# Kernel optimization log

Hardware: AMD Instinct MI355X
Metric: run time of the kernel (lower is better)

## Reference

```python
import jax, jax.numpy as jnp
import numpy as np

EPS = 1e-6

def _ln(x, g, b):
    mu = jnp.mean(x, axis=-1, keepdims=True)
    var = jnp.mean(jnp.square(x - mu), axis=-1, keepdims=True)
    return (x - mu) * jax.lax.rsqrt(var + EPS) * g + b

def setup_inputs() -> dict:
    key = jax.random.key(0)
    ks = jax.random.split(key, 8)
    B, S, D, H, HD, F = 4, 1024, 1024, 16, 64, 4096
    s = 0.02
    return {
        "hidden_state": jax.random.normal(ks[0], (B, S, D), jnp.float32),
        "mask": jnp.ones((B, S), jnp.int32),
        "Wq": jax.random.normal(ks[1], (H, D, HD), jnp.float32) * s,
        "bq": jnp.zeros((H, HD), jnp.float32),
        "Wk": jax.random.normal(ks[2], (H, D, HD), jnp.float32) * s,
        "bk": jnp.zeros((H, HD), jnp.float32),
        "Wv": jax.random.normal(ks[3], (H, D, HD), jnp.float32) * s,
        "bv": jnp.zeros((H, HD), jnp.float32),
        "Wo": jax.random.normal(ks[4], (D, D), jnp.float32) * s,
        "bo": jnp.zeros((D,), jnp.float32),
        "ln1_g": jnp.ones((D,), jnp.float32),
        "ln1_b": jnp.zeros((D,), jnp.float32),
        "ln2_g": jnp.ones((D,), jnp.float32),
        "ln2_b": jnp.zeros((D,), jnp.float32),
        "W1": jax.random.normal(ks[5], (D, F), jnp.float32) * s,
        "b1": jnp.zeros((F,), jnp.float32),
        "W2": jax.random.normal(ks[6], (F, D), jnp.float32) * s,
        "b2": jnp.zeros((D,), jnp.float32),
    }

def reference(hidden_state, mask, Wq, bq, Wk, bk, Wv, bv, Wo, bo,
              ln1_g, ln1_b, ln2_g, ln2_b, W1, b1, W2, b2):
    # Pre-norm
    x1 = _ln(hidden_state, ln1_g, ln1_b)  # [B,S,D]
    # Per-head projections stacked over head axis h
    q = jnp.einsum('bsd,hdk->bhsk', x1, Wq) + bq[:, None, :]
    k = jnp.einsum('bsd,hdk->bhsk', x1, Wk) + bk[:, None, :]
    v = jnp.einsum('bsd,hdk->bhsk', x1, Wv) + bv[:, None, :]
    head_dim = q.shape[-1]
    scores = jnp.einsum('bhqk,bhsk->bhqs', q, k) / jnp.sqrt(jnp.float32(head_dim))
    scores = jnp.where(mask[:, None, None, :] == 0, jnp.float32(-1e9), scores)
    w = jax.nn.softmax(scores, axis=-1)
    attn = jnp.einsum('bhqs,bhsk->bhqk', w, v)  # [B,H,S,HD]
    B, H, S, HD = attn.shape
    attn = attn.transpose(0, 2, 1, 3).reshape(B, S, H * HD)  # concat heads
    attn = attn @ Wo + bo
    h = attn + hidden_state
    x2 = _ln(h, ln2_g, ln2_b)
    ff = jax.nn.gelu(x2 @ W1 + b1, approximate=False) @ W2 + b2
    return ff + h
```

## Files before the change

### kernel.cpp

```cpp
#include <hip/hip_runtime.h>

typedef __bf16 bf16;
typedef __bf16 bf16x4 __attribute__((ext_vector_type(4)));
typedef __bf16 bf16x8 __attribute__((ext_vector_type(8)));
typedef float  f32x4  __attribute__((ext_vector_type(4)));

#define F32X4_ZERO ((f32x4){0.f, 0.f, 0.f, 0.f})

__device__ __forceinline__ f32x4 mfma16(bf16x8 a, bf16x8 b, f32x4 c) {
  return __builtin_amdgcn_mfma_f32_16x16x32_bf16(a, b, c, 0, 0, 0);
}

__device__ __forceinline__ void gld16(const void* g, void* l) {
  __builtin_amdgcn_global_load_lds((const __attribute__((address_space(1))) void*)g,
                                   (__attribute__((address_space(3))) void*)l, 16, 0, 0);
}

__device__ __forceinline__ float gelu_f(float u) {
  return 0.5f * u * (1.0f + erff(u * 0.70710678118654752f));
}

__device__ __forceinline__ bf16x8 frag_ld(const bf16* base, int row, int c16) {
  return *(const bf16x8*)((const char*)base + row * 128 + (((c16) ^ (row & 7)) << 4));
}

__device__ __forceinline__ bf16x8 frag_ld32(const bf16* base, int row, int c16) {
  return *(const bf16x8*)((const char*)base + row * 64 + ((c16 ^ ((row >> 1) & 3)) << 4));
}
#define WAITB(N) asm volatile("s_waitcnt vmcnt(" #N ")\ns_barrier" ::: "memory")

__global__ void transpose2(const float* __restrict__ src, size_t sBatch, int sStride,
                           bf16* __restrict__ dst, size_t dBatch, int dStride) {
  __shared__ bf16 t[32][33];
  src += (size_t)blockIdx.z * sBatch;
  dst += (size_t)blockIdx.z * dBatch;
  int c0 = blockIdx.x * 32, r0 = blockIdx.y * 32;
#pragma unroll
  for (int i = 0; i < 4; i++) {
    int r = threadIdx.y + i * 8;
    t[r][threadIdx.x] = (bf16)src[(size_t)(r0 + r) * sStride + c0 + threadIdx.x];
  }
  __syncthreads();
#pragma unroll
  for (int i = 0; i < 4; i++) {
    int c = threadIdx.y + i * 8;
    dst[(size_t)(c0 + c) * dStride + r0 + threadIdx.x] = t[threadIdx.x][c];
  }
}

__global__ __launch_bounds__(256) void ln_rows(const float* __restrict__ in,
                                               const float* __restrict__ gam,
                                               const float* __restrict__ bet,
                                               bf16* __restrict__ out) {
  int row = blockIdx.x, tid = threadIdx.x;
  f32x4 x = *(const f32x4*)(in + (size_t)row * 1024 + tid * 4);
  float s = 0.f, q = 0.f;
#pragma unroll
  for (int j = 0; j < 4; j++) { s += x[j]; q += x[j] * x[j]; }
#pragma unroll
  for (int o = 1; o < 64; o <<= 1) {
    s += __shfl_xor(s, o, 64);
    q += __shfl_xor(q, o, 64);
  }
  __shared__ float red[8];
  if ((tid & 63) == 0) { red[(tid >> 6) * 2] = s; red[(tid >> 6) * 2 + 1] = q; }
  __syncthreads();
  s = red[0] + red[2] + red[4] + red[6];
  q = red[1] + red[3] + red[5] + red[7];
  float mean = s * (1.f / 1024.f);
  float var  = q * (1.f / 1024.f) - mean * mean;
  float inv  = rsqrtf(var + 1e-6f);
  bf16x4 o;
#pragma unroll
  for (int j = 0; j < 4; j++) {
    int c = tid * 4 + j;
    o[j] = (bf16)((x[j] - mean) * inv * gam[c] + bet[c]);
  }
  *(bf16x4*)(out + (size_t)row * 1024 + tid * 4) = o;
}


__global__ __launch_bounds__(512) void pipe256_gelu(
    const bf16* __restrict__ A, const bf16* __restrict__ BT, const float* __restrict__ bias,
    int N, bf16* __restrict__ outb) {
  int tid = threadIdx.x, lane = tid & 63, wv = tid >> 6;
  int bid = blockIdx.x + (blockIdx.y << 4);
  int xcd = bid & 7, idx = bid >> 3;
  int m0 = ((xcd >> 1) * 4 + (idx >> 3)) * 256;
  int n0 = ((xcd & 1) * 8 + (idx & 7)) * 256;
  int wrow = (wv >> 2) * 128, wcol = (wv & 3) * 64;
  __shared__ __align__(16) bf16 lds[4][16384];
  f32x4 acc[8][4];
#pragma unroll
  for (int a = 0; a < 8; a++)
#pragma unroll
    for (int n = 0; n < 4; n++) acc[a][n] = F32X4_ZERO;

  constexpr int K = 1024, nk = K / 32;
  int rin = lane >> 2;
  int sbc = ((lane & 3) ^ ((lane >> 3) & 3)) * 16;
  auto stage = [&](int slot, int k0) {
#pragma unroll
    for (int j = 0; j < 4; j++) {
      int c = wv * 4 + j;
      if (c < 16)
        gld16((const char*)A + ((size_t)(m0 + c * 16 + rin) * K + k0) * 2 + sbc,
              (char*)lds[slot] + c * 1024);
      else
        gld16((const char*)BT + ((size_t)(n0 + (c - 16) * 16 + rin) * K + k0) * 2 + sbc,
              (char*)lds[slot] + c * 1024);
    }
  };

  stage(0, 0); stage(1, 32); stage(2, 64);
#pragma unroll 1
  for (int t = 0; t < nk; t++) {
    if (t < nk - 2)       WAITB(8);
    else if (t == nk - 2) WAITB(4);
    else                  WAITB(0);
    if (t + 3 < nk) stage((t + 3) & 3, (t + 3) * 32);
    const bf16* As = lds[t & 3];
    const bf16* Bs = lds[t & 3] + 8192;
    int c16 = lane >> 4;
    bf16x8 bfr[4];
#pragma unroll
    for (int nf = 0; nf < 4; nf++)
      bfr[nf] = frag_ld32(Bs, wcol + nf * 16 + (lane & 15), c16);
    __builtin_amdgcn_s_setprio(1);
#pragma unroll
    for (int mf = 0; mf < 8; mf++) {
      bf16x8 af = frag_ld32(As, wrow + mf * 16 + (lane & 15), c16);
#pragma unroll
      for (int nf = 0; nf < 4; nf++)
        acc[mf][nf] = mfma16(af, bfr[nf], acc[mf][nf]);
    }
    __builtin_amdgcn_s_setprio(0);
  }
#pragma unroll
  for (int mf = 0; mf < 8; mf++)
#pragma unroll
    for (int nf = 0; nf < 4; nf++)
#pragma unroll
      for (int i = 0; i < 4; i++) {
        int row = m0 + wrow + mf * 16 + ((lane >> 4) << 2) + i;
        int col = n0 + wcol + nf * 16 + (lane & 15);
        outb[(size_t)row * N + col] = (bf16)gelu_f(acc[mf][nf][i] + bias[col]);
      }
}

enum { EPI_WO = 0, EPI_GELU = 1, EPI_ACC0 = 2, EPI_ACC = 3, EPI_FINAL = 4 };

template <int EPI, int K>
__global__ __launch_bounds__(256) void pipe128(
    const bf16* __restrict__ A, const bf16* __restrict__ BT, const float* __restrict__ bias,
    int N,
    const float* __restrict__ resid, float* __restrict__ facc,
    bf16* __restrict__ outb, float* __restrict__ outf) {
  int tid = threadIdx.x, lane = tid & 63, wv = tid >> 6;
  int bid = blockIdx.x + (blockIdx.y << 3);
  int xcd = bid & 7, idx = bid >> 3;
  int m0 = (xcd * 4 + (idx >> 3)) * 128, n0 = (idx & 7) * 128;
  int wrow = (wv >> 1) * 64, wcol = (wv & 1) * 64;
  __shared__ __align__(16) bf16 lds[4][8192];
  f32x4 acc[4][4];
#pragma unroll
  for (int a = 0; a < 4; a++)
#pragma unroll
    for (int n = 0; n < 4; n++) acc[a][n] = F32X4_ZERO;

  constexpr int nk = K / 32;
  int rin = lane >> 2;
  int sbc = ((lane & 3) ^ ((lane >> 3) & 3)) * 16;
  auto stage = [&](int slot, int k0) {
#pragma unroll
    for (int j = 0; j < 4; j++) {
      int c = wv * 4 + j;
      if (c < 8)
        gld16((const char*)A + ((size_t)(m0 + c * 16 + rin) * K + k0) * 2 + sbc,
              (char*)lds[slot] + c * 1024);
      else
        gld16((const char*)BT + ((size_t)(n0 + (c - 8) * 16 + rin) * K + k0) * 2 + sbc,
              (char*)lds[slot] + c * 1024);
    }
  };

  stage(0, 0); stage(1, 32); stage(2, 64);
#pragma unroll 1
  for (int t = 0; t < nk; t++) {
    if (t < nk - 2)       WAITB(8);
    else if (t == nk - 2) WAITB(4);
    else                  WAITB(0);
    if (t + 3 < nk) stage((t + 3) & 3, (t + 3) * 32);
    const bf16* As = lds[t & 3];
    const bf16* Bs = lds[t & 3] + 4096;
    int c16 = lane >> 4;
    bf16x8 af[4], bfr[4];
#pragma unroll
    for (int mf = 0; mf < 4; mf++)
      af[mf] = frag_ld32(As, wrow + mf * 16 + (lane & 15), c16);
#pragma unroll
    for (int nf = 0; nf < 4; nf++)
      bfr[nf] = frag_ld32(Bs, wcol + nf * 16 + (lane & 15), c16);
    __builtin_amdgcn_s_setprio(1);
#pragma unroll
    for (int mf = 0; mf < 4; mf++)
#pragma unroll
      for (int nf = 0; nf < 4; nf++)
        acc[mf][nf] = mfma16(af[mf], bfr[nf], acc[mf][nf]);
    __builtin_amdgcn_s_setprio(0);
  }
#pragma unroll
  for (int mf = 0; mf < 4; mf++)
#pragma unroll
    for (int nf = 0; nf < 4; nf++)
#pragma unroll
      for (int i = 0; i < 4; i++) {
        int row = m0 + wrow + mf * 16 + ((lane >> 4) << 2) + i;
        int col = n0 + wcol + nf * 16 + (lane & 15);
        size_t idx2 = (size_t)row * N + col;
        float v = acc[mf][nf][i];
        if constexpr (EPI == EPI_WO) {
          outf[idx2] = v + bias[col] + resid[idx2];
        } else if constexpr (EPI == EPI_GELU) {
          outb[idx2] = (bf16)gelu_f(v + bias[col]);
        } else if constexpr (EPI == EPI_ACC0) {
          facc[idx2] = v;
        } else if constexpr (EPI == EPI_ACC) {
          facc[idx2] += v;
        } else {
          outf[idx2] = facc[idx2] + v + bias[col] + resid[idx2];
        }
      }
}

__global__ __launch_bounds__(256) void qkv_pipe(
    const bf16* __restrict__ x1,
    const bf16* __restrict__ WqT, const bf16* __restrict__ WkT, const bf16* __restrict__ WvT,
    const float* __restrict__ bq, const float* __restrict__ bk, const float* __restrict__ bv,
    bf16* __restrict__ qo, bf16* __restrict__ ko, bf16* __restrict__ vto) {
  int tid = threadIdx.x, lane = tid & 63, wv = tid >> 6;
  int z = blockIdx.z;
  const bf16* BT; const float* bias;
  if (z == 0)      { BT = WqT; bias = bq; }
  else if (z == 1) { BT = WkT; bias = bk; }
  else             { BT = WvT; bias = bv; }
  int bid = blockIdx.x + (blockIdx.y << 3);
  int xcd = bid & 7, idx = bid >> 3;
  int m0 = (xcd * 4 + (idx >> 3)) * 128, n0 = (idx & 7) * 128;
  int wrow = (wv >> 1) * 64, wcol = (wv & 1) * 64;
  __shared__ __align__(16) bf16 lds[4][8192];
  f32x4 acc[4][4];
#pragma unroll
  for (int a = 0; a < 4; a++)
#pragma unroll
    for (int n = 0; n < 4; n++) acc[a][n] = F32X4_ZERO;

  constexpr int K = 1024, nk = K / 32;
  int rin = lane >> 2;
  int sbc = ((lane & 3) ^ ((lane >> 3) & 3)) * 16;
  auto stage = [&](int slot, int k0) {
#pragma unroll
    for (int j = 0; j < 4; j++) {
      int c = wv * 4 + j;
      if (c < 8)
        gld16((const char*)x1 + ((size_t)(m0 + c * 16 + rin) * K + k0) * 2 + sbc,
              (char*)lds[slot] + c * 1024);
      else
        gld16((const char*)BT + ((size_t)(n0 + (c - 8) * 16 + rin) * K + k0) * 2 + sbc,
              (char*)lds[slot] + c * 1024);
    }
  };

  stage(0, 0); stage(1, 32); stage(2, 64);
#pragma unroll 1
  for (int t = 0; t < nk; t++) {
    if (t < nk - 2)       WAITB(8);
    else if (t == nk - 2) WAITB(4);
    else                  WAITB(0);
    if (t + 3 < nk) stage((t + 3) & 3, (t + 3) * 32);
    const bf16* As = lds[t & 3];
    const bf16* Bs = lds[t & 3] + 4096;
    int c16 = lane >> 4;
    bf16x8 af[4], bfr[4];
#pragma unroll
    for (int mf = 0; mf < 4; mf++)
      af[mf] = frag_ld32(As, wrow + mf * 16 + (lane & 15), c16);
#pragma unroll
    for (int nf = 0; nf < 4; nf++)
      bfr[nf] = frag_ld32(Bs, wcol + nf * 16 + (lane & 15), c16);
    __builtin_amdgcn_s_setprio(1);
#pragma unroll
    for (int mf = 0; mf < 4; mf++)
#pragma unroll
      for (int nf = 0; nf < 4; nf++)
        acc[mf][nf] = mfma16(af[mf], bfr[nf], acc[mf][nf]);
    __builtin_amdgcn_s_setprio(0);
  }
#pragma unroll
  for (int mf = 0; mf < 4; mf++)
#pragma unroll
    for (int nf = 0; nf < 4; nf++)
#pragma unroll
      for (int i = 0; i < 4; i++) {
        int row  = m0 + wrow + mf * 16 + ((lane >> 4) << 2) + i;
        int ncol = n0 + wcol + nf * 16 + (lane & 15);
        int bb = row >> 10, s = row & 1023, head = ncol >> 6, d = ncol & 63;
        size_t bh = (size_t)bb * 16 + head;
        float v = acc[mf][nf][i] + bias[ncol];
        if (z == 0)      qo[(bh * 1024 + s) * 64 + d] = (bf16)(v * 0.125f);
        else if (z == 1) ko[(bh * 1024 + s) * 64 + d] = (bf16)v;
        else             vto[(bh * 64 + d) * 1024 + s] = (bf16)v;
      }
}

__global__ __launch_bounds__(512) void attn_flash(
    const bf16* __restrict__ qb, const bf16* __restrict__ kb, const bf16* __restrict__ vtb,
    const int* __restrict__ mask, bf16* __restrict__ attnC) {
  int tid = threadIdx.x, lane = tid & 63, wv = tid >> 6;
  int wgid = blockIdx.x;
  int nid  = (wgid & 7) * 64 + (wgid >> 3);
  int qblk = nid & 7, h = (nid >> 3) & 15, b = nid >> 7;
  int qrow0 = qblk * 128 + wv * 16;

  __shared__ float smask[1024];
  __shared__ __align__(16) bf16 kt[2][64 * 64];
  __shared__ __align__(16) bf16 vt[2][64 * 64];
  __shared__ __align__(16) bf16 pb[8][16][72];
  for (int i = tid; i < 1024; i += 512) smask[i] = mask[b * 1024 + i] ? 0.f : -1e9f;

  size_t bh = (size_t)b * 16 + h;
  const bf16* qp = qb + (bh * 1024 + qrow0) * 64;
  bf16x8 qa[2];
#pragma unroll
  for (int kc = 0; kc < 2; kc++)
    qa[kc] = *(const bf16x8*)(qp + (lane & 15) * 64 + kc * 32 + (lane >> 4) * 8);

  const bf16* kp = kb + bh * 1024 * 64;
  const bf16* vp = vtb + bh * 64 * 1024;
  bf16* myp = &pb[wv][0][0];

  bf16x8 vone;
#pragma unroll
  for (int j = 0; j < 8; j++) vone[j] = (bf16)1.0f;

  f32x4 ssum = F32X4_ZERO;
  f32x4 oacc[4];
#pragma unroll
  for (int i = 0; i < 4; i++) oacc[i] = F32X4_ZERO;

  int srl = lane >> 3;
  int sbc = ((lane & 7) ^ srl) * 16;
  auto stage = [&](int buf, int t2) {
    int key0n = t2 * 64;
#pragma unroll
    for (int j = 0; j < 2; j++) {
      int c = wv * 2 + j;
      if (c < 8) {
        int row = c * 8 + srl;
        gld16((const char*)kp + ((size_t)(key0n + row) * 64) * 2 + sbc,
              (char*)kt[buf] + c * 1024);
      } else {
        int row = (c - 8) * 8 + srl;
        gld16((const char*)vp + ((size_t)row * 1024 + key0n) * 2 + sbc,
              (char*)vt[buf] + (c - 8) * 1024);
      }
    }
  };

  stage(0, 0);
  __syncthreads();

  for (int t = 0; t < 16; t++) {
    int cur = t & 1;
    if (t < 15) stage(cur ^ 1, t + 1);
    const bf16* kcur = kt[cur];
    const bf16* vcur = vt[cur];
    int key0 = t * 64;
    f32x4 st[4];
    __builtin_amdgcn_s_setprio(1);
#pragma unroll
    for (int nt = 0; nt < 4; nt++) {
      st[nt] = F32X4_ZERO;
#pragma unroll
      for (int kc = 0; kc < 2; kc++) {
        bf16x8 kf = frag_ld(kcur, nt * 16 + (lane & 15), kc * 4 + (lane >> 4));
        st[nt] = mfma16(qa[kc], kf, st[nt]);
      }
    }
    __builtin_amdgcn_s_setprio(0);
#pragma unroll
    for (int nt = 0; nt < 4; nt++) {
      float ms = smask[key0 + nt * 16 + (lane & 15)] - 8.0f;
#pragma unroll
      for (int i = 0; i < 4; i++) st[nt][i] = __expf(st[nt][i] + ms);
    }
#pragma unroll
    for (int nt = 0; nt < 4; nt++)
#pragma unroll
      for (int i = 0; i < 4; i++)
        myp[((lane >> 4) * 4 + i) * 72 + nt * 16 + (lane & 15)] = (bf16)st[nt][i];
    __builtin_amdgcn_s_setprio(1);
#pragma unroll
    for (int kc = 0; kc < 2; kc++) {
      bf16x8 pa = *(const bf16x8*)(myp + (lane & 15) * 72 + kc * 32 + (lane >> 4) * 8);
      ssum = mfma16(pa, vone, ssum);
#pragma unroll
      for (int dn = 0; dn < 4; dn++) {
        bf16x8 vf = frag_ld(vcur, dn * 16 + (lane & 15), kc * 4 + (lane >> 4));
        oacc[dn] = mfma16(pa, vf, oacc[dn]);
      }
    }
    __builtin_amdgcn_s_setprio(0);
    __syncthreads();
  }
#pragma unroll
  for (int i = 0; i < 4; i++) {
    float inv = 1.0f / ssum[i];
    int row = qrow0 + ((lane >> 4) << 2) + i;
#pragma unroll
    for (int dn = 0; dn < 4; dn++)
      attnC[(size_t)(b * 1024 + row) * 1024 + h * 64 + dn * 16 + (lane & 15)] =
          (bf16)(oacc[dn][i] * inv);
  }
}

template <int EPI, int K>
__global__ __launch_bounds__(256) void gemm_bt(
    const bf16* __restrict__ A, const bf16* __restrict__ BT, const float* __restrict__ bias,
    int N,
    const float* __restrict__ resid, float* __restrict__ facc,
    bf16* __restrict__ outb, float* __restrict__ outf) {
  int tid = threadIdx.x, lane = tid & 63, wv = tid >> 6;
  int m0 = blockIdx.y * 128, n0 = blockIdx.x * 128;
  int wrow = (wv >> 1) * 64, wcol = (wv & 1) * 64;
  __shared__ __align__(16) bf16 lA[2][128 * 64];
  __shared__ __align__(16) bf16 lB[2][128 * 64];
  f32x4 acc[4][4];
#pragma unroll
  for (int a = 0; a < 4; a++)
#pragma unroll
    for (int n = 0; n < 4; n++) acc[a][n] = F32X4_ZERO;

  int cbs = ((lane & 7) ^ (lane >> 3)) * 16;
  auto stage = [&](int buf, int k0) {
#pragma unroll
    for (int s = 0; s < 4; s++) {
      int c = s * 4 + wv;
      int row = c * 8 + (lane >> 3);
      gld16((const char*)A  + ((size_t)(m0 + row) * K + k0) * 2 + cbs,
            (char*)lA[buf] + c * 1024);
      gld16((const char*)BT + ((size_t)(n0 + row) * K + k0) * 2 + cbs,
            (char*)lB[buf] + c * 1024);
    }
  };

  constexpr int nk = K >> 6;
  stage(0, 0);
  __syncthreads();
#pragma unroll 1
  for (int t = 0; t < nk; t++) {
    int cur = t & 1;
    if (t + 1 < nk) stage(cur ^ 1, (t + 1) * 64);
#pragma unroll
    for (int kc = 0; kc < 2; kc++) {
      int c16 = kc * 4 + (lane >> 4);
      bf16x8 af[4], bfr[4];
#pragma unroll
      for (int mf = 0; mf < 4; mf++)
        af[mf] = frag_ld(lA[cur], wrow + mf * 16 + (lane & 15), c16);
#pragma unroll
      for (int nf = 0; nf < 4; nf++)
        bfr[nf] = frag_ld(lB[cur], wcol + nf * 16 + (lane & 15), c16);
#pragma unroll
      for (int mf = 0; mf < 4; mf++)
#pragma unroll
        for (int nf = 0; nf < 4; nf++)
          acc[mf][nf] = mfma16(af[mf], bfr[nf], acc[mf][nf]);
    }
    __syncthreads();
  }
#pragma unroll
  for (int mf = 0; mf < 4; mf++)
#pragma unroll
    for (int nf = 0; nf < 4; nf++)
#pragma unroll
      for (int i = 0; i < 4; i++) {
        int row = m0 + wrow + mf * 16 + ((lane >> 4) << 2) + i;
        int col = n0 + wcol + nf * 16 + (lane & 15);
        size_t idx2 = (size_t)row * N + col;
        float v = acc[mf][nf][i];
        if constexpr (EPI == EPI_WO) {
          outf[idx2] = v + bias[col] + resid[idx2];
        } else if constexpr (EPI == EPI_GELU) {
          outb[idx2] = (bf16)gelu_f(v + bias[col]);
        } else if constexpr (EPI == EPI_ACC0) {
          facc[idx2] = v;
        } else if constexpr (EPI == EPI_ACC) {
          facc[idx2] += v;
        } else {
          outf[idx2] = facc[idx2] + v + bias[col] + resid[idx2];
        }
      }
}

extern "C" void kernel_launch(void* const* d_in, const int* in_sizes, int n_in,
                              void* d_out, int out_size, void* d_ws, size_t ws_size,
                              hipStream_t stream) {
  const float* hidden = (const float*)d_in[0];
  const int*   mask   = (const int*)d_in[1];
  const float* Wq = (const float*)d_in[2];
  const float* bq = (const float*)d_in[3];
  const float* Wk = (const float*)d_in[4];
  const float* bk = (const float*)d_in[5];
  const float* Wv = (const float*)d_in[6];
  const float* bv = (const float*)d_in[7];
  const float* Wo = (const float*)d_in[8];
  const float* bo = (const float*)d_in[9];
  const float* ln1g = (const float*)d_in[10];
  const float* ln1b = (const float*)d_in[11];
  const float* ln2g = (const float*)d_in[12];
  const float* ln2b = (const float*)d_in[13];
  const float* W1 = (const float*)d_in[14];
  const float* b1 = (const float*)d_in[15];
  const float* W2 = (const float*)d_in[16];
  const float* b2 = (const float*)d_in[17];
  float* out = (float*)d_out;

  char* ws = (char*)d_ws;
  const size_t MB = 1ull << 20;
  dim3 tb(32, 8);
  const size_t HB = 64 * 1024;

  if (ws_size >= 96 * MB) {
    bf16* x1    = (bf16*)(ws + 0 * MB);
    bf16* attnC = x1;
    bf16* x2    = x1;
    bf16* qbuf  = (bf16*)(ws + 8 * MB);
    bf16* W1T   = qbuf;
    bf16* kbuf  = (bf16*)(ws + 16 * MB);
    bf16* W2T   = kbuf;
    bf16* vtbuf = (bf16*)(ws + 24 * MB);
    float* hbuf = (float*)(ws + 32 * MB);
    bf16* WqT   = (bf16*)(ws + 48 * MB);
    bf16* WkT   = (bf16*)(ws + 50 * MB);
    bf16* WvT   = (bf16*)(ws + 52 * MB);
    bf16* WoT   = (bf16*)(ws + 54 * MB);
    bf16* gbuf  = (bf16*)(ws + 56 * MB);

    transpose2<<<dim3(2, 32, 16), tb, 0, stream>>>(Wq, HB, 64, WqT, HB, 1024);
    transpose2<<<dim3(2, 32, 16), tb, 0, stream>>>(Wk, HB, 64, WkT, HB, 1024);
    transpose2<<<dim3(2, 32, 16), tb, 0, stream>>>(Wv, HB, 64, WvT, HB, 1024);
    transpose2<<<dim3(32, 32, 1), tb, 0, stream>>>(Wo, 0, 1024, WoT, 0, 1024);
    ln_rows<<<4096, 256, 0, stream>>>(hidden, ln1g, ln1b, x1);
    qkv_pipe<<<dim3(8, 32, 3), 256, 0, stream>>>(x1, WqT, WkT, WvT, bq, bk, bv,
                                                 qbuf, kbuf, vtbuf);
    attn_flash<<<512, 512, 0, stream>>>(qbuf, kbuf, vtbuf, mask, attnC);
    pipe128<EPI_WO, 1024><<<dim3(8, 32), 256, 0, stream>>>(attnC, WoT, bo, 1024,
                                                           hidden, nullptr, nullptr, hbuf);
    ln_rows<<<4096, 256, 0, stream>>>(hbuf, ln2g, ln2b, x2);
    transpose2<<<dim3(128, 32, 1), tb, 0, stream>>>(W1, 0, 4096, W1T, 0, 1024);
    transpose2<<<dim3(32, 128, 1), tb, 0, stream>>>(W2, 0, 1024, W2T, 0, 4096);
    pipe256_gelu<<<dim3(16, 16), 512, 0, stream>>>(x2, W1T, b1, 4096, gbuf);
    pipe128<EPI_WO, 4096><<<dim3(8, 32), 256, 0, stream>>>(gbuf, W2T, b2, 1024,
                                                           hbuf, nullptr, nullptr, out);
  } else {
    bf16* x1     = (bf16*)(ws + 0 * MB);
    bf16* attnC  = x1;
    bf16* x2     = x1;
    bf16* qbuf   = (bf16*)(ws + 8 * MB);
    bf16* W1Tc   = (bf16*)(ws + 8 * MB);
    bf16* W2Tc   = (bf16*)(ws + 10 * MB);
    bf16* gchunk = (bf16*)(ws + 12 * MB);
    bf16* kbuf   = (bf16*)(ws + 16 * MB);
    bf16* vtbuf  = (bf16*)(ws + 24 * MB);
    float* hbuf  = (float*)(ws + 16 * MB);
    bf16* WqT    = (bf16*)(ws + 32 * MB);
    bf16* WkT    = (bf16*)(ws + 34 * MB);
    bf16* WvT    = (bf16*)(ws + 36 * MB);
    bf16* WoT    = (bf16*)(ws + 38 * MB);
    float* outacc = (float*)(ws + 40 * MB);

    transpose2<<<dim3(2, 32, 16), tb, 0, stream>>>(Wq, HB, 64, WqT, HB, 1024);
    transpose2<<<dim3(2, 32, 16), tb, 0, stream>>>(Wk, HB, 64, WkT, HB, 1024);
    transpose2<<<dim3(2, 32, 16), tb, 0, stream>>>(Wv, HB, 64, WvT, HB, 1024);
    transpose2<<<dim3(32, 32, 1), tb, 0, stream>>>(Wo, 0, 1024, WoT, 0, 1024);
    ln_rows<<<4096, 256, 0, stream>>>(hidden, ln1g, ln1b, x1);
    qkv_pipe<<<dim3(8, 32, 3), 256, 0, stream>>>(x1, WqT, WkT, WvT, bq, bk, bv,
                                                 qbuf, kbuf, vtbuf);
    attn_flash<<<512, 512, 0, stream>>>(qbuf, kbuf, vtbuf, mask, attnC);
    pipe128<EPI_WO, 1024><<<dim3(8, 32), 256, 0, stream>>>(attnC, WoT, bo, 1024,
                                                           hidden, nullptr, nullptr, hbuf);
    ln_rows<<<4096, 256, 0, stream>>>(hbuf, ln2g, ln2b, x2);

    for (int c = 0; c < 8; c++) {
      transpose2<<<dim3(16, 32, 1), tb, 0, stream>>>(W1 + c * 512, 0, 4096,
                                                     W1Tc, 0, 1024);
      transpose2<<<dim3(32, 16, 1), tb, 0, stream>>>(W2 + (size_t)c * 512 * 1024, 0, 1024,
                                                     W2Tc, 0, 512);
      gemm_bt<EPI_GELU, 1024><<<dim3(4, 32), 256, 0, stream>>>(x2, W1Tc, b1 + c * 512, 512,
                                                               nullptr, nullptr, gchunk, nullptr);
      if (c == 0)
        gemm_bt<EPI_ACC0, 512><<<dim3(8, 32), 256, 0, stream>>>(gchunk, W2Tc, b2, 1024,
                                                                nullptr, outacc, nullptr, nullptr);
      else if (c < 7)
        gemm_bt<EPI_ACC, 512><<<dim3(8, 32), 256, 0, stream>>>(gchunk, W2Tc, b2, 1024,
                                                               nullptr, outacc, nullptr, nullptr);
      else
        gemm_bt<EPI_FINAL, 512><<<dim3(8, 32), 256, 0, stream>>>(gchunk, W2Tc, b2, 1024,
                                                                 hbuf, outacc, nullptr, out);
    }
  }

  (void)in_sizes; (void)n_in; (void)out_size;
}
```

Baseline: 263.3 us.

## Replace 256-tile GELU GEMM with 128-tile pipe and shrink LDS ring to three stages

```diff
diff --git a/kernel.cpp b/kernel.cpp
--- a/kernel.cpp
+++ b/kernel.cpp
@@ -79,78 +79,9 @@
   *(bf16x4*)(out + (size_t)row * 1024 + tid * 4) = o;
 }
 
-
-__global__ __launch_bounds__(512) void pipe256_gelu(
-    const bf16* __restrict__ A, const bf16* __restrict__ BT, const float* __restrict__ bias,
-    int N, bf16* __restrict__ outb) {
-  int tid = threadIdx.x, lane = tid & 63, wv = tid >> 6;
-  int bid = blockIdx.x + (blockIdx.y << 4);
-  int xcd = bid & 7, idx = bid >> 3;
-  int m0 = ((xcd >> 1) * 4 + (idx >> 3)) * 256;
-  int n0 = ((xcd & 1) * 8 + (idx & 7)) * 256;
-  int wrow = (wv >> 2) * 128, wcol = (wv & 3) * 64;
-  __shared__ __align__(16) bf16 lds[4][16384];
-  f32x4 acc[8][4];
-#pragma unroll
-  for (int a = 0; a < 8; a++)
-#pragma unroll
-    for (int n = 0; n < 4; n++) acc[a][n] = F32X4_ZERO;
-
-  constexpr int K = 1024, nk = K / 32;
-  int rin = lane >> 2;
-  int sbc = ((lane & 3) ^ ((lane >> 3) & 3)) * 16;
-  auto stage = [&](int slot, int k0) {
-#pragma unroll
-    for (int j = 0; j < 4; j++) {
-      int c = wv * 4 + j;
-      if (c < 16)
-        gld16((const char*)A + ((size_t)(m0 + c * 16 + rin) * K + k0) * 2 + sbc,
-              (char*)lds[slot] + c * 1024);
-      else
-        gld16((const char*)BT + ((size_t)(n0 + (c - 16) * 16 + rin) * K + k0) * 2 + sbc,
-              (char*)lds[slot] + c * 1024);
-    }
-  };
-
-  stage(0, 0); stage(1, 32); stage(2, 64);
-#pragma unroll 1
-  for (int t = 0; t < nk; t++) {
-    if (t < nk - 2)       WAITB(8);
-    else if (t == nk - 2) WAITB(4);
-    else                  WAITB(0);
-    if (t + 3 < nk) stage((t + 3) & 3, (t + 3) * 32);
-    const bf16* As = lds[t & 3];
-    const bf16* Bs = lds[t & 3] + 8192;
-    int c16 = lane >> 4;
-    bf16x8 bfr[4];
-#pragma unroll
-    for (int nf = 0; nf < 4; nf++)
-      bfr[nf] = frag_ld32(Bs, wcol + nf * 16 + (lane & 15), c16);
-    __builtin_amdgcn_s_setprio(1);
-#pragma unroll
-    for (int mf = 0; mf < 8; mf++) {
-      bf16x8 af = frag_ld32(As, wrow + mf * 16 + (lane & 15), c16);
-#pragma unroll
-      for (int nf = 0; nf < 4; nf++)
-        acc[mf][nf] = mfma16(af, bfr[nf], acc[mf][nf]);
-    }
-    __builtin_amdgcn_s_setprio(0);
-  }
-#pragma unroll
-  for (int mf = 0; mf < 8; mf++)
-#pragma unroll
-    for (int nf = 0; nf < 4; nf++)
-#pragma unroll
-      for (int i = 0; i < 4; i++) {
-        int row = m0 + wrow + mf * 16 + ((lane >> 4) << 2) + i;
-        int col = n0 + wcol + nf * 16 + (lane & 15);
-        outb[(size_t)row * N + col] = (bf16)gelu_f(acc[mf][nf][i] + bias[col]);
-      }
-}
-
 enum { EPI_WO = 0, EPI_GELU = 1, EPI_ACC0 = 2, EPI_ACC = 3, EPI_FINAL = 4 };
 
-template <int EPI, int K>
+template <int EPI, int K, int NTL>
 __global__ __launch_bounds__(256) void pipe128(
     const bf16* __restrict__ A, const bf16* __restrict__ BT, const float* __restrict__ bias,
     int N,
@@ -159,9 +90,10 @@
   int tid = threadIdx.x, lane = tid & 63, wv = tid >> 6;
   int bid = blockIdx.x + (blockIdx.y << 3);
   int xcd = bid & 7, idx = bid >> 3;
-  int m0 = (xcd * 4 + (idx >> 3)) * 128, n0 = (idx & 7) * 128;
+  int m0 = (xcd * 4 + (idx >> NTL)) * 128;
+  int n0 = (idx & ((1 << NTL) - 1)) * 128;
   int wrow = (wv >> 1) * 64, wcol = (wv & 1) * 64;
-  __shared__ __align__(16) bf16 lds[4][8192];
+  __shared__ __align__(16) bf16 lds[3][8192];
   f32x4 acc[4][4];
 #pragma unroll
   for (int a = 0; a < 4; a++)
@@ -184,15 +116,14 @@
     }
   };
 
-  stage(0, 0); stage(1, 32); stage(2, 64);
+  stage(0, 0); stage(1, 32);
 #pragma unroll 1
   for (int t = 0; t < nk; t++) {
-    if (t < nk - 2)       WAITB(8);
-    else if (t == nk - 2) WAITB(4);
-    else                  WAITB(0);
-    if (t + 3 < nk) stage((t + 3) & 3, (t + 3) * 32);
-    const bf16* As = lds[t & 3];
-    const bf16* Bs = lds[t & 3] + 4096;
+    if (t < nk - 1) WAITB(4);
+    else            WAITB(0);
+    if (t + 2 < nk) stage((t + 2) % 3, (t + 2) * 32);
+    const bf16* As = lds[t % 3];
+    const bf16* Bs = lds[t % 3] + 4096;
     int c16 = lane >> 4;
     bf16x8 af[4], bfr[4];
 #pragma unroll
@@ -201,13 +132,11 @@
 #pragma unroll
     for (int nf = 0; nf < 4; nf++)
       bfr[nf] = frag_ld32(Bs, wcol + nf * 16 + (lane & 15), c16);
-    __builtin_amdgcn_s_setprio(1);
 #pragma unroll
     for (int mf = 0; mf < 4; mf++)
 #pragma unroll
       for (int nf = 0; nf < 4; nf++)
         acc[mf][nf] = mfma16(af[mf], bfr[nf], acc[mf][nf]);
-    __builtin_amdgcn_s_setprio(0);
   }
 #pragma unroll
   for (int mf = 0; mf < 4; mf++)
@@ -248,7 +177,7 @@
   int xcd = bid & 7, idx = bid >> 3;
   int m0 = (xcd * 4 + (idx >> 3)) * 128, n0 = (idx & 7) * 128;
   int wrow = (wv >> 1) * 64, wcol = (wv & 1) * 64;
-  __shared__ __align__(16) bf16 lds[4][8192];
+  __shared__ __align__(16) bf16 lds[3][8192];
   f32x4 acc[4][4];
 #pragma unroll
   for (int a = 0; a < 4; a++)
@@ -271,15 +200,14 @@
     }
   };
 
-  stage(0, 0); stage(1, 32); stage(2, 64);
+  stage(0, 0); stage(1, 32);
 #pragma unroll 1
   for (int t = 0; t < nk; t++) {
-    if (t < nk - 2)       WAITB(8);
-    else if (t == nk - 2) WAITB(4);
-    else                  WAITB(0);
-    if (t + 3 < nk) stage((t + 3) & 3, (t + 3) * 32);
-    const bf16* As = lds[t & 3];
-    const bf16* Bs = lds[t & 3] + 4096;
+    if (t < nk - 1) WAITB(4);
+    else            WAITB(0);
+    if (t + 2 < nk) stage((t + 2) % 3, (t + 2) * 32);
+    const bf16* As = lds[t % 3];
+    const bf16* Bs = lds[t % 3] + 4096;
     int c16 = lane >> 4;
     bf16x8 af[4], bfr[4];
 #pragma unroll
@@ -288,13 +216,11 @@
 #pragma unroll
     for (int nf = 0; nf < 4; nf++)
       bfr[nf] = frag_ld32(Bs, wcol + nf * 16 + (lane & 15), c16);
-    __builtin_amdgcn_s_setprio(1);
 #pragma unroll
     for (int mf = 0; mf < 4; mf++)
 #pragma unroll
       for (int nf = 0; nf < 4; nf++)
         acc[mf][nf] = mfma16(af[mf], bfr[nf], acc[mf][nf]);
-    __builtin_amdgcn_s_setprio(0);
   }
 #pragma unroll
   for (int mf = 0; mf < 4; mf++)
@@ -555,14 +481,15 @@
     qkv_pipe<<<dim3(8, 32, 3), 256, 0, stream>>>(x1, WqT, WkT, WvT, bq, bk, bv,
                                                  qbuf, kbuf, vtbuf);
     attn_flash<<<512, 512, 0, stream>>>(qbuf, kbuf, vtbuf, mask, attnC);
-    pipe128<EPI_WO, 1024><<<dim3(8, 32), 256, 0, stream>>>(attnC, WoT, bo, 1024,
-                                                           hidden, nullptr, nullptr, hbuf);
+    pipe128<EPI_WO, 1024, 3><<<dim3(8, 32), 256, 0, stream>>>(attnC, WoT, bo, 1024,
+                                                              hidden, nullptr, nullptr, hbuf);
     ln_rows<<<4096, 256, 0, stream>>>(hbuf, ln2g, ln2b, x2);
     transpose2<<<dim3(128, 32, 1), tb, 0, stream>>>(W1, 0, 4096, W1T, 0, 1024);
     transpose2<<<dim3(32, 128, 1), tb, 0, stream>>>(W2, 0, 1024, W2T, 0, 4096);
-    pipe256_gelu<<<dim3(16, 16), 512, 0, stream>>>(x2, W1T, b1, 4096, gbuf);
-    pipe128<EPI_WO, 4096><<<dim3(8, 32), 256, 0, stream>>>(gbuf, W2T, b2, 1024,
-                                                           hbuf, nullptr, nullptr, out);
+    pipe128<EPI_GELU, 1024, 5><<<dim3(8, 128), 256, 0, stream>>>(x2, W1T, b1, 4096,
+                                                                 nullptr, nullptr, gbuf, nullptr);
+    pipe128<EPI_WO, 4096, 3><<<dim3(8, 32), 256, 0, stream>>>(gbuf, W2T, b2, 1024,
+                                                              hbuf, nullptr, nullptr, out);
   } else {
     bf16* x1     = (bf16*)(ws + 0 * MB);
     bf16* attnC  = x1;
@@ -588,8 +515,8 @@
     qkv_pipe<<<dim3(8, 32, 3), 256, 0, stream>>>(x1, WqT, WkT, WvT, bq, bk, bv,
                                                  qbuf, kbuf, vtbuf);
     attn_flash<<<512, 512, 0, stream>>>(qbuf, kbuf, vtbuf, mask, attnC);
-    pipe128<EPI_WO, 1024><<<dim3(8, 32), 256, 0, stream>>>(attnC, WoT, bo, 1024,
-                                                           hidden, nullptr, nullptr, hbuf);
+    pipe128<EPI_WO, 1024, 3><<<dim3(8, 32), 256, 0, stream>>>(attnC, WoT, bo, 1024,
+                                                              hidden, nullptr, nullptr, hbuf);
     ln_rows<<<4096, 256, 0, stream>>>(hbuf, ln2g, ln2b, x2);
 
     for (int c = 0; c < 8; c++) {
```

Result: faster. 231.4 us (-12.1%).
